# Optimization experiments

Measured on AMD Instinct MI355X. Metric: run time of the kernel, lower is better.

Reference implementation:

```python
import jax, jax.numpy as jnp
import numpy as np

H = 32; D = 128; HID = 4096       # heads, head_dim, hidden
DOFF = 1024; BD = 32; T = DOFF + BD  # prefill tokens, decode batch, total tokens
MAXKV = 513; R = 16; NA = 4       # kv-cache slots, lora rank, num adapters
SCALE = 1.0 / float(np.sqrt(D))


def _add_lora(y, x, wa, wb, segment):
    # segmented (multi-tenant) LoRA: y[t] += x[t] @ A[aid(t)] @ B[aid(t)]
    t = x.shape[0]
    aid = jnp.clip(jnp.searchsorted(segment, jnp.arange(t), side='right') - 1, 0, NA - 1)
    oh = jax.nn.one_hot(aid, NA, dtype=x.dtype)           # [t, NA]
    u = jnp.einsum('th,ahr->atr', x, wa)                  # [NA, t, R]
    v = jnp.einsum('atr,arh->ath', u, wb)                 # [NA, t, HID]
    return y + jnp.einsum('ta,ath->th', oh, v)


def setup_inputs() -> dict:
    key = jax.random.key(0)
    ks = jax.random.split(key, 16)
    f = lambda k, s: (jax.random.normal(k, s, dtype=jnp.float32) * 0.02)
    inp = {
        'hidden_states': f(ks[0], (T, HID)),
        'Wq': f(ks[1], (HID, HID)), 'Wk': f(ks[2], (HID, HID)),
        'Wv': f(ks[3], (HID, HID)), 'Wo': f(ks[4], (HID, HID)),
        'wa_q': f(ks[5], (NA, HID, R)), 'wb_q': f(ks[6], (NA, R, HID)),
        'wa_k': f(ks[7], (NA, HID, R)), 'wb_k': f(ks[8], (NA, R, HID)),
        'wa_v': f(ks[9], (NA, HID, R)), 'wb_v': f(ks[10], (NA, R, HID)),
        'wa_o': f(ks[11], (NA, HID, R)), 'wb_o': f(ks[12], (NA, R, HID)),
        'k_cache': f(ks[13], (BD, MAXKV, H, D)),
        'v_cache': f(ks[14], (BD, MAXKV, H, D)),
        'indptr': jnp.array([0, 200, 456, 800, 1024], dtype=jnp.int32),
        'segment': jnp.array([0, 300, 600, 900, 1056], dtype=jnp.int32),
        'kv_lens': jax.random.randint(ks[15], (BD,), 0, 512, dtype=jnp.int32),
    }
    return inp


def reference(hidden_states, Wq, Wk, Wv, Wo, wa_q, wb_q, wa_k, wb_k, wa_v, wb_v,
              wa_o, wb_o, k_cache, v_cache, indptr, segment, kv_lens):
    # qkv proj + segmented LoRA add
    qp = _add_lora(hidden_states @ Wq, hidden_states, wa_q, wb_q, segment)
    kp = _add_lora(hidden_states @ Wk, hidden_states, wa_k, wb_k, segment)
    vp = _add_lora(hidden_states @ Wv, hidden_states, wa_v, wb_v, segment)

    # ---- ragged prefill attention (causal within each sequence) ----
    q = qp[:DOFF].reshape(DOFF, H, D)
    k = kp[:DOFF].reshape(DOFF, H, D)
    v = vp[:DOFF].reshape(DOFF, H, D)
    idx = jnp.arange(DOFF)
    seg = jnp.searchsorted(indptr, idx, side='right') - 1   # sequence id per token
    m = (seg[:, None] == seg[None, :]) & (idx[None, :] <= idx[:, None])
    s = jnp.einsum('qhd,khd->hqk', q, k) * SCALE
    p = jax.nn.softmax(jnp.where(m[None], s, -1e9), axis=-1)
    out_p = jnp.einsum('hqk,khd->qhd', p, v).reshape(DOFF, HID)

    # ---- paged decode attention (append new kv, attend over cache) ----
    qd = qp[DOFF:].reshape(BD, H, D)
    kd = kp[DOFF:].reshape(BD, H, D)
    vd = vp[DOFF:].reshape(BD, H, D)
    b = jnp.arange(BD)
    kc = k_cache.at[b, kv_lens].set(kd)
    vc = v_cache.at[b, kv_lens].set(vd)
    lens = kv_lens + 1
    md = jnp.arange(MAXKV)[None, :] < lens[:, None]          # [BD, MAXKV]
    sd = jnp.einsum('bhd,bkhd->bhk', qd, kc) * SCALE
    pd = jax.nn.softmax(jnp.where(md[:, None, :], sd, -1e9), axis=-1)
    out_d = jnp.einsum('bhk,bkhd->bhd', pd, vc).reshape(BD, HID)

    attn = jnp.concatenate([out_p, out_d], axis=0)           # [T, HID]
    o = _add_lora(attn @ Wo, attn, wa_o, wb_o, segment)
    return o
```

## Files before the change

kernel.cpp:

```cpp
#include <hip/hip_runtime.h>
#include <hip/hip_bf16.h>

#define H_     32
#define D_     128
#define HID_   4096
#define DOFF_  1024
#define BD_    32
#define T_     1056
#define MAXKV_ 513
#define R_     16
#define NA_    4
#define SCALE_ 0.08838834764831845f

typedef __attribute__((ext_vector_type(8))) short short8;
typedef __attribute__((ext_vector_type(4))) float f32x4;

__device__ __forceinline__ float toF(float x) { return x; }
__device__ __forceinline__ float toF(__hip_bfloat16 x) { return __bfloat162float(x); }
__device__ __forceinline__ void storev(float* p, float v) { *p = v; }
__device__ __forceinline__ void storev(__hip_bfloat16* p, float v) { *p = __float2bfloat16(v); }

__device__ __forceinline__ void gload16(const void* g, void* l) {
  __builtin_amdgcn_global_load_lds(
      (const __attribute__((address_space(1))) unsigned int*)g,
      (__attribute__((address_space(3))) unsigned int*)l, 16, 0, 0);
}

__device__ __forceinline__ void load4(const float* p, float* v) {
  float4 t = *(const float4*)p;
  v[0] = t.x; v[1] = t.y; v[2] = t.z; v[3] = t.w;
}
__device__ __forceinline__ void load4(const __hip_bfloat16* p, float* v) {
  short4 t = *(const short4*)p;
  const __hip_bfloat16* e = (const __hip_bfloat16*)&t;
  v[0] = toF(e[0]); v[1] = toF(e[1]); v[2] = toF(e[2]); v[3] = toF(e[3]);
}

__global__ __launch_bounds__(256) void cast_bf16_kernel(
    const float* __restrict__ X, __hip_bfloat16* __restrict__ Y, int n4) {
  int i = blockIdx.x * 256 + threadIdx.x;
  if (i >= n4) return;
  float4 v = ((const float4*)X)[i];
  __hip_bfloat16 o[4] = {__float2bfloat16(v.x), __float2bfloat16(v.y),
                         __float2bfloat16(v.z), __float2bfloat16(v.w)};
  *(short4*)(Y + (size_t)i * 4) = *(short4*)o;
}

__global__ __launch_bounds__(256) void transpose_cast_kernel(
    const float* __restrict__ W, __hip_bfloat16* __restrict__ WT) {
  __shared__ float tile[64][65];
  int tx = threadIdx.x & 15;
  int ty = threadIdx.x >> 4;
  int r0 = blockIdx.y * 64, c0 = blockIdx.x * 64;
#pragma unroll
  for (int s = 0; s < 64; s += 16) {
    float4 v = *(const float4*)(W + (size_t)(r0 + ty + s) * HID_ + c0 + tx * 4);
    tile[ty + s][tx * 4 + 0] = v.x;
    tile[ty + s][tx * 4 + 1] = v.y;
    tile[ty + s][tx * 4 + 2] = v.z;
    tile[ty + s][tx * 4 + 3] = v.w;
  }
  __syncthreads();
#pragma unroll
  for (int s = 0; s < 64; s += 16) {
    int c = ty + s;
    __hip_bfloat16 o[4];
#pragma unroll
    for (int e = 0; e < 4; ++e) o[e] = __float2bfloat16(tile[tx * 4 + e][c]);
    *(short4*)(WT + (size_t)(c0 + c) * HID_ + r0 + tx * 4) = *(short4*)o;
  }
}

template <typename XT>
__global__ __launch_bounds__(256) void lora_u_kernel(
    const XT* __restrict__ X, const float* __restrict__ WA0,
    const float* __restrict__ WA1, const float* __restrict__ WA2,
    const int* __restrict__ segment, float* __restrict__ U0,
    float* __restrict__ U1, float* __restrict__ U2) {
  int t = blockIdx.x;
  int tid = threadIdx.x;
  const float* WA = blockIdx.y == 0 ? WA0 : (blockIdx.y == 1 ? WA1 : WA2);
  float* U = blockIdx.y == 0 ? U0 : (blockIdx.y == 1 ? U1 : U2);

  int aid = 0;
#pragma unroll
  for (int i = 1; i < NA_; ++i)
    if (t >= segment[i]) aid = i;

  const XT* x = X + (size_t)t * HID_;
  const float* wa = WA + (size_t)aid * HID_ * R_;

  float part[R_];
#pragma unroll
  for (int r = 0; r < R_; ++r) part[r] = 0.f;

  for (int h = tid * 4; h < HID_; h += 1024) {
    float xv[4];
    load4(x + h, xv);
#pragma unroll
    for (int e = 0; e < 4; ++e) {
      const float* w = wa + (size_t)(h + e) * R_;
#pragma unroll
      for (int r = 0; r < R_; ++r) part[r] += xv[e] * w[r];
    }
  }

  __shared__ float red[256][R_ + 1];
#pragma unroll
  for (int r = 0; r < R_; ++r) red[tid][r] = part[r];
  __syncthreads();
  for (int s = 128; s > 0; s >>= 1) {
    if (tid < s) {
#pragma unroll
      for (int r = 0; r < R_; ++r) red[tid][r] += red[tid + s][r];
    }
    __syncthreads();
  }
  if (tid < R_) U[(size_t)t * R_ + tid] = red[0][tid];
}

template <typename OUT_T>
__global__ __launch_bounds__(256) void gemm_bf16_lora_kernel(
    const __hip_bfloat16* __restrict__ Xb, const __hip_bfloat16* __restrict__ WT,
    const float* __restrict__ U, const float* __restrict__ BMAT,
    const int* __restrict__ segment, OUT_T* __restrict__ Y, int Trows) {
  __shared__ __hip_bfloat16 As[64 * 32];
  __shared__ __hip_bfloat16 Bs[128 * 32];

  const int tid = threadIdx.x;
  const int lane = tid & 63;
  const int wave = tid >> 6;
  const int wr = (wave >> 1) * 32;
  const int wc = (wave & 1) * 64;
  const int m0 = blockIdx.y * 64, n0 = blockIdx.x * 128;

  const int srow = tid >> 2;
  const int sel = (tid & 3) * 8;
  int ar0 = m0 + srow; if (ar0 >= Trows) ar0 = Trows - 1;
  const __hip_bfloat16* gA0 = Xb + (size_t)ar0 * HID_ + sel;
  const __hip_bfloat16* gB0 = WT + (size_t)(n0 + srow) * HID_ + sel;
  const __hip_bfloat16* gB1 = WT + (size_t)(n0 + srow + 64) * HID_ + sel;
  __hip_bfloat16* lA = As + tid * 8;
  __hip_bfloat16* lB = Bs + tid * 8;

  const int lrow = lane & 15;
  const int lk = (lane >> 4) * 8;
  const __hip_bfloat16* fA = As + (wr + lrow) * 32 + lk;
  const __hip_bfloat16* fB = Bs + (wc + lrow) * 32 + lk;

  f32x4 acc[2][4] = {};

  for (int k0 = 0; k0 < HID_; k0 += 32) {
    gload16(gA0, lA);
    gload16(gB0, lB);
    gload16(gB1, lB + 2048);
    gA0 += 32; gB0 += 32; gB1 += 32;
    __syncthreads();
    short8 a[2], b[4];
#pragma unroll
    for (int mi = 0; mi < 2; ++mi) a[mi] = *(const short8*)(fA + mi * 512);
#pragma unroll
    for (int ni = 0; ni < 4; ++ni) b[ni] = *(const short8*)(fB + ni * 512);
#pragma unroll
    for (int mi = 0; mi < 2; ++mi)
#pragma unroll
      for (int ni = 0; ni < 4; ++ni)
        acc[mi][ni] = __builtin_amdgcn_mfma_f32_16x16x32_bf16(a[mi], b[ni], acc[mi][ni], 0, 0, 0);
    __syncthreads();
  }

  const int crow = (lane >> 4) * 4;
  const int ccol = lane & 15;
#pragma unroll
  for (int mi = 0; mi < 2; ++mi) {
    const int tb = m0 + wr + mi * 16 + crow;
#pragma unroll
    for (int i = 0; i < 4; ++i) {
      const int t = tb + i;
      if (t >= Trows) continue;
      int aid = 0;
#pragma unroll
      for (int s = 1; s < NA_; ++s)
        if (t >= segment[s]) aid = s;
      const float* ub = U + (size_t)t * R_;
      const float* bb = BMAT + (size_t)aid * R_ * HID_;
#pragma unroll
      for (int ni = 0; ni < 4; ++ni) {
        const int n = n0 + wc + ni * 16 + ccol;
        float v = acc[mi][ni][i];
        const float* bc = bb + n;
#pragma unroll
        for (int r = 0; r < R_; ++r) v += ub[r] * bc[(size_t)r * HID_];
        storev(Y + (size_t)t * HID_ + n, v);
      }
    }
  }
}

#define QB 64
#define KB 32

__global__ __launch_bounds__(256) void attn_prefill_mfma_kernel(
    const __hip_bfloat16* __restrict__ qp, const __hip_bfloat16* __restrict__ kp,
    const __hip_bfloat16* __restrict__ vp, const int* __restrict__ indptr,
    __hip_bfloat16* __restrict__ attn) {
  __shared__ __hip_bfloat16 Klds[KB * 128];
  __shared__ __hip_bfloat16 Vt[128 * 40];
  __shared__ __hip_bfloat16 Plds[4][16 * 40];

  const int tid = threadIdx.x;
  const int lane = tid & 63;
  const int wave = tid >> 6;
  const int g = lane >> 4;
  const int lc = lane & 15;
  const int q0 = blockIdx.x * QB;
  const int h = blockIdx.y;

  int qrows[4], qstart[4];
#pragma unroll
  for (int i = 0; i < 4; ++i) {
    int q = q0 + wave * 16 + g * 4 + i;
    qrows[i] = q;
    int s0 = 0;
#pragma unroll
    for (int j = 1; j < NA_; ++j)
      if (q >= indptr[j]) s0 = indptr[j];
    qstart[i] = s0;
  }

  short8 aq[4];
  {
    const __hip_bfloat16* qrow = qp + (size_t)(q0 + wave * 16 + lc) * HID_ + h * D_;
#pragma unroll
    for (int dc = 0; dc < 4; ++dc)
      aq[dc] = *(const short8*)(qrow + dc * 32 + g * 8);
  }

  float mrow[4], lrow[4];
#pragma unroll
  for (int i = 0; i < 4; ++i) { mrow[i] = -1e30f; lrow[i] = 0.f; }
  f32x4 o[8] = {};

  int ks0 = 0;
#pragma unroll
  for (int j = 1; j < NA_; ++j)
    if (q0 >= indptr[j]) ks0 = indptr[j];
  const int kt0 = ks0 & ~(KB - 1);

  const int sr = tid >> 4;
  const int sc = tid & 15;

  for (int kt = kt0; kt < q0 + QB; kt += KB) {
    gload16(kp + (size_t)(kt + sr) * HID_ + h * D_ + ((sc ^ (sr & 7)) * 8),
            Klds + tid * 8);
    gload16(kp + (size_t)(kt + 16 + sr) * HID_ + h * D_ + ((sc ^ (sr & 7)) * 8),
            Klds + 2048 + tid * 8);
    {
      short8 v0 = *(const short8*)(vp + (size_t)(kt + sr) * HID_ + h * D_ + sc * 8);
      short8 v1 = *(const short8*)(vp + (size_t)(kt + 16 + sr) * HID_ + h * D_ + sc * 8);
      const __hip_bfloat16* e0 = (const __hip_bfloat16*)&v0;
      const __hip_bfloat16* e1 = (const __hip_bfloat16*)&v1;
#pragma unroll
      for (int e = 0; e < 8; ++e) {
        Vt[(sc * 8 + e) * 40 + sr] = e0[e];
        Vt[(sc * 8 + e) * 40 + sr + 16] = e1[e];
      }
    }
    __syncthreads();

    f32x4 s0v = {}, s1v = {};
#pragma unroll
    for (int dc = 0; dc < 4; ++dc) {
      const int cb = dc * 4 + g;
      short8 bk0 = *(const short8*)(Klds + lc * 128 + ((cb ^ (lc & 7)) * 8));
      short8 bk1 = *(const short8*)(Klds + (16 + lc) * 128 + ((cb ^ (lc & 7)) * 8));
      s0v = __builtin_amdgcn_mfma_f32_16x16x32_bf16(aq[dc], bk0, s0v, 0, 0, 0);
      s1v = __builtin_amdgcn_mfma_f32_16x16x32_bf16(aq[dc], bk1, s1v, 0, 0, 0);
    }

    const int kl0 = kt + lc, kl1 = kt + 16 + lc;
#pragma unroll
    for (int i = 0; i < 4; ++i) {
      float sm0 = s0v[i] * SCALE_;
      float sm1 = s1v[i] * SCALE_;
      bool v0ok = (kl0 >= qstart[i]) && (kl0 <= qrows[i]);
      bool v1ok = (kl1 >= qstart[i]) && (kl1 <= qrows[i]);
      float mx = fmaxf(v0ok ? sm0 : -1e30f, v1ok ? sm1 : -1e30f);
#pragma unroll
      for (int off = 1; off < 16; off <<= 1)
        mx = fmaxf(mx, __shfl_xor(mx, off));
      float mnew = fmaxf(mrow[i], mx);
      float alpha = __expf(mrow[i] - mnew);
      float p0 = v0ok ? __expf(sm0 - mnew) : 0.f;
      float p1 = v1ok ? __expf(sm1 - mnew) : 0.f;
      lrow[i] = lrow[i] * alpha + p0 + p1;
      mrow[i] = mnew;
#pragma unroll
      for (int dc = 0; dc < 8; ++dc) o[dc][i] *= alpha;
      Plds[wave][(g * 4 + i) * 40 + lc] = __float2bfloat16(p0);
      Plds[wave][(g * 4 + i) * 40 + 16 + lc] = __float2bfloat16(p1);
    }

    asm volatile("s_waitcnt lgkmcnt(0)" ::: "memory");

    short8 ap = *(const short8*)(&Plds[wave][lc * 40 + g * 8]);
#pragma unroll
    for (int dc = 0; dc < 8; ++dc) {
      short8 bv = *(const short8*)(&Vt[(dc * 16 + lc) * 40 + g * 8]);
      o[dc] = __builtin_amdgcn_mfma_f32_16x16x32_bf16(ap, bv, o[dc], 0, 0, 0);
    }
    __syncthreads();
  }

#pragma unroll
  for (int i = 0; i < 4; ++i) {
    float l = lrow[i];
#pragma unroll
    for (int off = 1; off < 16; off <<= 1) l += __shfl_xor(l, off);
    lrow[i] = 1.f / l;
  }
#pragma unroll
  for (int dc = 0; dc < 8; ++dc)
#pragma unroll
    for (int i = 0; i < 4; ++i)
      attn[(size_t)qrows[i] * HID_ + h * D_ + dc * 16 + lc] =
          __float2bfloat16(o[dc][i] * lrow[i]);
}

__global__ __launch_bounds__(256) void attn_decode_kernel(
    const __hip_bfloat16* __restrict__ qp, const __hip_bfloat16* __restrict__ kp,
    const __hip_bfloat16* __restrict__ vp, const float* __restrict__ kcache,
    const float* __restrict__ vcache, const int* __restrict__ kv_lens,
    __hip_bfloat16* __restrict__ attn) {
  int h = blockIdx.x;
  int b = blockIdx.y;
  int wave = threadIdx.x >> 6;
  int lane = threadIdx.x & 63;
  int t = DOFF_ + b;

  const __hip_bfloat16* qptr = qp + (size_t)t * HID_ + h * D_;
  float q0 = toF(qptr[lane]), q1 = toF(qptr[lane + 64]);
  int len = kv_lens[b];

  int cnt = len + 1;
  int chunk = (cnt + 3) >> 2;
  int ks = wave * chunk;
  int ke = ks + chunk; if (ke > cnt) ke = cnt;

  float m = -1e30f, l = 0.f, acc0 = 0.f, acc1 = 0.f;
  for (int k = ks; k < ke; ++k) {
    float kv0, kv1, vv0, vv1;
    if (k == len) {
      const __hip_bfloat16* kptr = kp + (size_t)t * HID_ + h * D_;
      const __hip_bfloat16* vptr = vp + (size_t)t * HID_ + h * D_;
      kv0 = toF(kptr[lane]); kv1 = toF(kptr[lane + 64]);
      vv0 = toF(vptr[lane]); vv1 = toF(vptr[lane + 64]);
    } else {
      size_t base = (((size_t)b * MAXKV_ + k) * H_ + h) * D_;
      kv0 = kcache[base + lane]; kv1 = kcache[base + lane + 64];
      vv0 = vcache[base + lane]; vv1 = vcache[base + lane + 64];
    }
    float s = q0 * kv0 + q1 * kv1;
#pragma unroll
    for (int off = 32; off > 0; off >>= 1) s += __shfl_xor(s, off);
    s *= SCALE_;
    float mnew = fmaxf(m, s);
    float alpha = __expf(m - mnew);
    float p = __expf(s - mnew);
    acc0 = acc0 * alpha + p * vv0;
    acc1 = acc1 * alpha + p * vv1;
    l = l * alpha + p;
    m = mnew;
  }

  __shared__ float sm[4], sl[4], sacc[4][128];
  if (lane == 0) { sm[wave] = m; sl[wave] = l; }
  sacc[wave][lane] = acc0;
  sacc[wave][lane + 64] = acc1;
  __syncthreads();
  if (wave == 0) {
    float M = fmaxf(fmaxf(sm[0], sm[1]), fmaxf(sm[2], sm[3]));
    float L = 0.f, A0 = 0.f, A1 = 0.f;
#pragma unroll
    for (int w = 0; w < 4; ++w) {
      float sc = __expf(sm[w] - M);
      L += sl[w] * sc;
      A0 += sacc[w][lane] * sc;
      A1 += sacc[w][lane + 64] * sc;
    }
    float inv = 1.f / L;
    __hip_bfloat16* outp = attn + (size_t)t * HID_ + h * D_;
    storev(outp + lane, A0 * inv);
    storev(outp + lane + 64, A1 * inv);
  }
}

extern "C" void kernel_launch(void* const* d_in, const int* in_sizes, int n_in,
                              void* d_out, int out_size, void* d_ws, size_t ws_size,
                              hipStream_t stream) {
  const float* hidden  = (const float*)d_in[0];
  const float* Wq      = (const float*)d_in[1];
  const float* Wk      = (const float*)d_in[2];
  const float* Wv      = (const float*)d_in[3];
  const float* Wo      = (const float*)d_in[4];
  const float* wa_q    = (const float*)d_in[5];
  const float* wb_q    = (const float*)d_in[6];
  const float* wa_k    = (const float*)d_in[7];
  const float* wb_k    = (const float*)d_in[8];
  const float* wa_v    = (const float*)d_in[9];
  const float* wb_v    = (const float*)d_in[10];
  const float* wa_o    = (const float*)d_in[11];
  const float* wb_o    = (const float*)d_in[12];
  const float* k_cache = (const float*)d_in[13];
  const float* v_cache = (const float*)d_in[14];
  const int*   indptr  = (const int*)d_in[15];
  const int*   segment = (const int*)d_in[16];
  const int*   kv_lens = (const int*)d_in[17];
  float* out = (float*)d_out;

  const size_t PROJ = (size_t)T_ * HID_;
  __hip_bfloat16* Xb    = (__hip_bfloat16*)d_ws;
  __hip_bfloat16* qp    = Xb + PROJ;
  __hip_bfloat16* kp    = qp + PROJ;
  __hip_bfloat16* vp    = kp + PROJ;
  __hip_bfloat16* attnb = vp + PROJ;
  __hip_bfloat16* WT    = attnb + PROJ;
  float* u_q = (float*)(WT + (size_t)HID_ * HID_);
  float* u_k = u_q + (size_t)T_ * R_;
  float* u_v = u_k + (size_t)T_ * R_;
  float* u_o = u_v + (size_t)T_ * R_;

  const int n4 = (int)(PROJ / 4);
  dim3 tg(HID_ / 64, HID_ / 64);
  dim3 gg(HID_ / 128, (T_ + 63) / 64);

  cast_bf16_kernel<<<(n4 + 255) / 256, 256, 0, stream>>>(hidden, Xb, n4);
  lora_u_kernel<float><<<dim3(T_, 3), 256, 0, stream>>>(
      hidden, wa_q, wa_k, wa_v, segment, u_q, u_k, u_v);

  transpose_cast_kernel<<<tg, 256, 0, stream>>>(Wq, WT);
  gemm_bf16_lora_kernel<__hip_bfloat16><<<gg, 256, 0, stream>>>(Xb, WT, u_q, wb_q, segment, qp, T_);
  transpose_cast_kernel<<<tg, 256, 0, stream>>>(Wk, WT);
  gemm_bf16_lora_kernel<__hip_bfloat16><<<gg, 256, 0, stream>>>(Xb, WT, u_k, wb_k, segment, kp, T_);
  transpose_cast_kernel<<<tg, 256, 0, stream>>>(Wv, WT);
  gemm_bf16_lora_kernel<__hip_bfloat16><<<gg, 256, 0, stream>>>(Xb, WT, u_v, wb_v, segment, vp, T_);

  attn_prefill_mfma_kernel<<<dim3(DOFF_ / QB, H_), 256, 0, stream>>>(qp, kp, vp, indptr, attnb);
  attn_decode_kernel<<<dim3(H_, BD_), 256, 0, stream>>>(qp, kp, vp, k_cache, v_cache,
                                                        kv_lens, attnb);

  lora_u_kernel<__hip_bfloat16><<<dim3(T_, 1), 256, 0, stream>>>(
      attnb, wa_o, wa_o, wa_o, segment, u_o, u_o, u_o);
  transpose_cast_kernel<<<tg, 256, 0, stream>>>(Wo, WT);
  gemm_bf16_lora_kernel<float><<<gg, 256, 0, stream>>>(attnb, WT, u_o, wb_o, segment, out, T_);
}
```

Measured before the change: 777.7 us.

## Batch weight transposes, fuse QKV GEMMs, enlarge GEMM tile, swizzle workgroups

The four weight transpose-casts now run as one launch over a z-dimension into a 4x larger workspace. The Q/K/V projections become a single GEMM launch that selects the weight, U, B and output by column block. The GEMM tile grows from 64x128 to 128x128, so each wave computes 4x4 MFMA tiles. A workgroup-index swizzle is added to both the GEMM and the prefill attention to improve L2 locality. This reduces launch count and A-tile reloads and fills the GPU better, at the cost of more registers per wave, more workspace memory and some wasted rows in the final partial M tile.

```diff
diff --git a/kernel.cpp b/kernel.cpp
--- a/kernel.cpp
+++ b/kernel.cpp
@@ -46,9 +46,14 @@
   *(short4*)(Y + (size_t)i * 4) = *(short4*)o;
 }
 
-__global__ __launch_bounds__(256) void transpose_cast_kernel(
-    const float* __restrict__ W, __hip_bfloat16* __restrict__ WT) {
+__global__ __launch_bounds__(256) void transpose_cast4_kernel(
+    const float* __restrict__ W0, const float* __restrict__ W1,
+    const float* __restrict__ W2, const float* __restrict__ W3,
+    __hip_bfloat16* __restrict__ WT4) {
   __shared__ float tile[64][65];
+  const float* W = blockIdx.z == 0 ? W0 : (blockIdx.z == 1 ? W1
+                   : (blockIdx.z == 2 ? W2 : W3));
+  __hip_bfloat16* WT = WT4 + (size_t)blockIdx.z * HID_ * HID_;
   int tx = threadIdx.x & 15;
   int ty = threadIdx.x >> 4;
   int r0 = blockIdx.y * 64, c0 = blockIdx.x * 64;
@@ -121,23 +126,41 @@
 
 template <typename OUT_T>
 __global__ __launch_bounds__(256) void gemm_bf16_lora_kernel(
-    const __hip_bfloat16* __restrict__ Xb, const __hip_bfloat16* __restrict__ WT,
-    const float* __restrict__ U, const float* __restrict__ BMAT,
-    const int* __restrict__ segment, OUT_T* __restrict__ Y, int Trows) {
-  __shared__ __hip_bfloat16 As[64 * 32];
+    const __hip_bfloat16* __restrict__ Xb, const __hip_bfloat16* __restrict__ WT4,
+    const float* __restrict__ U0, const float* __restrict__ U1,
+    const float* __restrict__ U2, const float* __restrict__ B0,
+    const float* __restrict__ B1, const float* __restrict__ B2,
+    const int* __restrict__ segment, OUT_T* __restrict__ Y0,
+    OUT_T* __restrict__ Y1, OUT_T* __restrict__ Y2, int Trows) {
+  __shared__ __hip_bfloat16 As[128 * 32];
   __shared__ __hip_bfloat16 Bs[128 * 32];
+
+  const int nwg = gridDim.x * gridDim.y;
+  const int flat = blockIdx.y * gridDim.x + blockIdx.x;
+  const int swz = (flat & 7) * (nwg >> 3) + (flat >> 3);
+  const int bx = swz % gridDim.x;
+  const int by = swz / gridDim.x;
+  const int w = bx >> 5;
+  const int n0 = (bx & 31) * 128;
+  const int m0 = by * 128;
+
+  const __hip_bfloat16* WT = WT4 + (size_t)w * HID_ * HID_;
+  const float* U = w == 0 ? U0 : (w == 1 ? U1 : U2);
+  const float* BMAT = w == 0 ? B0 : (w == 1 ? B1 : B2);
+  OUT_T* Y = w == 0 ? Y0 : (w == 1 ? Y1 : Y2);
 
   const int tid = threadIdx.x;
   const int lane = tid & 63;
   const int wave = tid >> 6;
-  const int wr = (wave >> 1) * 32;
+  const int wr = (wave >> 1) * 64;
   const int wc = (wave & 1) * 64;
-  const int m0 = blockIdx.y * 64, n0 = blockIdx.x * 128;
 
   const int srow = tid >> 2;
   const int sel = (tid & 3) * 8;
-  int ar0 = m0 + srow; if (ar0 >= Trows) ar0 = Trows - 1;
+  int ar0 = m0 + srow;      if (ar0 >= Trows) ar0 = Trows - 1;
+  int ar1 = m0 + srow + 64; if (ar1 >= Trows) ar1 = Trows - 1;
   const __hip_bfloat16* gA0 = Xb + (size_t)ar0 * HID_ + sel;
+  const __hip_bfloat16* gA1 = Xb + (size_t)ar1 * HID_ + sel;
   const __hip_bfloat16* gB0 = WT + (size_t)(n0 + srow) * HID_ + sel;
   const __hip_bfloat16* gB1 = WT + (size_t)(n0 + srow + 64) * HID_ + sel;
   __hip_bfloat16* lA = As + tid * 8;
@@ -148,21 +171,22 @@
   const __hip_bfloat16* fA = As + (wr + lrow) * 32 + lk;
   const __hip_bfloat16* fB = Bs + (wc + lrow) * 32 + lk;
 
-  f32x4 acc[2][4] = {};
+  f32x4 acc[4][4] = {};
 
   for (int k0 = 0; k0 < HID_; k0 += 32) {
     gload16(gA0, lA);
+    gload16(gA1, lA + 2048);
     gload16(gB0, lB);
     gload16(gB1, lB + 2048);
-    gA0 += 32; gB0 += 32; gB1 += 32;
+    gA0 += 32; gA1 += 32; gB0 += 32; gB1 += 32;
     __syncthreads();
-    short8 a[2], b[4];
-#pragma unroll
-    for (int mi = 0; mi < 2; ++mi) a[mi] = *(const short8*)(fA + mi * 512);
+    short8 a[4], b[4];
+#pragma unroll
+    for (int mi = 0; mi < 4; ++mi) a[mi] = *(const short8*)(fA + mi * 512);
 #pragma unroll
     for (int ni = 0; ni < 4; ++ni) b[ni] = *(const short8*)(fB + ni * 512);
 #pragma unroll
-    for (int mi = 0; mi < 2; ++mi)
+    for (int mi = 0; mi < 4; ++mi)
 #pragma unroll
       for (int ni = 0; ni < 4; ++ni)
         acc[mi][ni] = __builtin_amdgcn_mfma_f32_16x16x32_bf16(a[mi], b[ni], acc[mi][ni], 0, 0, 0);
@@ -172,7 +196,7 @@
   const int crow = (lane >> 4) * 4;
   const int ccol = lane & 15;
 #pragma unroll
-  for (int mi = 0; mi < 2; ++mi) {
+  for (int mi = 0; mi < 4; ++mi) {
     const int tb = m0 + wr + mi * 16 + crow;
 #pragma unroll
     for (int i = 0; i < 4; ++i) {
@@ -208,13 +232,17 @@
   __shared__ __hip_bfloat16 Vt[128 * 40];
   __shared__ __hip_bfloat16 Plds[4][16 * 40];
 
+  const int nwg = gridDim.x * gridDim.y;
+  const int flat = blockIdx.y * gridDim.x + blockIdx.x;
+  const int swz = (flat & 7) * (nwg >> 3) + (flat >> 3);
+  const int q0 = (swz % gridDim.x) * QB;
+  const int h = swz / gridDim.x;
+
   const int tid = threadIdx.x;
   const int lane = tid & 63;
   const int wave = tid >> 6;
   const int g = lane >> 4;
   const int lc = lane & 15;
-  const int q0 = blockIdx.x * QB;
-  const int h = blockIdx.y;
 
   int qrows[4], qstart[4];
 #pragma unroll
@@ -424,26 +452,22 @@
   __hip_bfloat16* kp    = qp + PROJ;
   __hip_bfloat16* vp    = kp + PROJ;
   __hip_bfloat16* attnb = vp + PROJ;
-  __hip_bfloat16* WT    = attnb + PROJ;
-  float* u_q = (float*)(WT + (size_t)HID_ * HID_);
+  __hip_bfloat16* WT4   = attnb + PROJ;
+  float* u_q = (float*)(WT4 + 4 * (size_t)HID_ * HID_);
   float* u_k = u_q + (size_t)T_ * R_;
   float* u_v = u_k + (size_t)T_ * R_;
   float* u_o = u_v + (size_t)T_ * R_;
 
   const int n4 = (int)(PROJ / 4);
-  dim3 tg(HID_ / 64, HID_ / 64);
-  dim3 gg(HID_ / 128, (T_ + 63) / 64);
 
   cast_bf16_kernel<<<(n4 + 255) / 256, 256, 0, stream>>>(hidden, Xb, n4);
+  transpose_cast4_kernel<<<dim3(HID_ / 64, HID_ / 64, 4), 256, 0, stream>>>(
+      Wq, Wk, Wv, Wo, WT4);
   lora_u_kernel<float><<<dim3(T_, 3), 256, 0, stream>>>(
       hidden, wa_q, wa_k, wa_v, segment, u_q, u_k, u_v);
 
-  transpose_cast_kernel<<<tg, 256, 0, stream>>>(Wq, WT);
-  gemm_bf16_lora_kernel<__hip_bfloat16><<<gg, 256, 0, stream>>>(Xb, WT, u_q, wb_q, segment, qp, T_);
-  transpose_cast_kernel<<<tg, 256, 0, stream>>>(Wk, WT);
-  gemm_bf16_lora_kernel<__hip_bfloat16><<<gg, 256, 0, stream>>>(Xb, WT, u_k, wb_k, segment, kp, T_);
-  transpose_cast_kernel<<<tg, 256, 0, stream>>>(Wv, WT);
-  gemm_bf16_lora_kernel<__hip_bfloat16><<<gg, 256, 0, stream>>>(Xb, WT, u_v, wb_v, segment, vp, T_);
+  gemm_bf16_lora_kernel<__hip_bfloat16><<<dim3(96, 9), 256, 0, stream>>>(
+      Xb, WT4, u_q, u_k, u_v, wb_q, wb_k, wb_v, segment, qp, kp, vp, T_);
 
   attn_prefill_mfma_kernel<<<dim3(DOFF_ / QB, H_), 256, 0, stream>>>(qp, kp, vp, indptr, attnb);
   attn_decode_kernel<<<dim3(H_, BD_), 256, 0, stream>>>(qp, kp, vp, k_cache, v_cache,
@@ -451,6 +475,7 @@
 
   lora_u_kernel<__hip_bfloat16><<<dim3(T_, 1), 256, 0, stream>>>(
       attnb, wa_o, wa_o, wa_o, segment, u_o, u_o, u_o);
-  transpose_cast_kernel<<<tg, 256, 0, stream>>>(Wo, WT);
-  gemm_bf16_lora_kernel<float><<<gg, 256, 0, stream>>>(attnb, WT, u_o, wb_o, segment, out, T_);
-}
+  gemm_bf16_lora_kernel<float><<<dim3(32, 9), 256, 0, stream>>>(
+      attnb, WT4 + 3 * (size_t)HID_ * HID_, u_o, u_o, u_o, wb_o, wb_o, wb_o,
+      segment, out, out, out, T_);
+}
```

Result: faster. 751.7 us (-3.4%).
